# Kernel tuning notes

Hardware: AMD Instinct MI355X
Metric: run time of the kernel (lower is better)

Reference implementation:

```python
import jax, jax.numpy as jnp
import numpy as np

N, K, P, A, NBINS, RP = 4096, 48, 128, 5, 16, 32
LN_EPS = 1e-5

def _normalize(v, eps=1e-6):
    return v / jnp.sqrt(jnp.maximum((v * v).sum(-1, keepdims=True), eps))

def extract_frames(pos):
    # pos: [N, A, 3]; atom order N, CA, C, ... -> Gram-Schmidt backbone frame
    n, ca, c = pos[:, 0], pos[:, 1], pos[:, 2]
    e1 = _normalize(c - ca)
    v2 = n - ca
    e2 = _normalize(v2 - (v2 * e1).sum(-1, keepdims=True) * e1)
    e3 = jnp.cross(e1, e2)
    R = jnp.stack([e1, e2, e3], axis=-1)  # [N,3,3], columns = frame axes
    return R, ca

def distance_rbf(d, d_min=0.0, d_max=22.0, bins=NBINS):
    step = (d_max - d_min) / bins
    centers = d_min + step * jnp.arange(bins, dtype=d.dtype)
    return jnp.exp(-(((d[..., None] - centers) / step) ** 2))

def relpos_features(resi, chain, batch, neighbours):
    # clipped relative sequence position, extra class for cross-chain/batch pairs
    rel = jnp.clip(resi[neighbours] - resi[:, None], -RP, RP) + RP
    same = (chain[neighbours] == chain[:, None]) & (batch[neighbours] == batch[:, None])
    cls = jnp.where(same, rel, 2 * RP + 1)
    return jax.nn.one_hot(cls, 2 * RP + 2, dtype=jnp.float32)  # [N,K,66]

def distance_features(pos, neighbours):
    pn = pos[neighbours]  # [N,K,A,3] gather
    diff = pos[:, None, :, None] - pn[:, :, None, :]  # [N,K,A,A,3]
    d = jnp.sqrt(jnp.maximum((diff * diff).sum(-1), 1e-12))
    return distance_rbf(d).reshape(N, K, A * A * NBINS)

def direction_features(pos, neighbours, R, ca):
    rel = pos[neighbours] - ca[:, None, None]  # [N,K,A,3]
    local = jnp.einsum('nji,nkaj->nkai', R, rel)  # express in frame of residue i
    return _normalize(local).reshape(N, K, A * 3)

def rotation_features(neighbours, R):
    Rrel = jnp.einsum('nji,nkjl->nkil', R, R[neighbours])  # R_i^T R_j
    return Rrel.reshape(N, K, 9)

def pair_vector_features(pos, neighbours, R, ca):
    rel = pos[neighbours] - ca[:, None, None]
    local = jnp.einsum('nji,nkaj->nkai', R, rel)
    return local.reshape(N, K, A * 3)

def setup_inputs() -> dict:
    key = jax.random.key(0)
    ks = jax.random.split(key, 12)
    s = 0.02
    pos = 5.0 * jax.random.normal(ks[0], (N, A, 3), dtype=jnp.float32)
    dmap = 22.0 * jax.random.uniform(ks[1], (N, N), dtype=jnp.float32)
    mask = jnp.ones((N,), dtype=jnp.float32)
    neighbours = jax.random.randint(ks[2], (N, K), 0, N, dtype=jnp.int32)
    resi = jnp.arange(N, dtype=jnp.int32)
    chain = jnp.zeros((N,), dtype=jnp.int32)
    batch = jnp.zeros((N,), dtype=jnp.int32)
    W_relpos = s * jax.random.normal(ks[3], (2 * RP + 2, P), dtype=jnp.float32)
    W_dmap = s * jax.random.normal(ks[4], (NBINS, P), dtype=jnp.float32)
    W_dist = s * jax.random.normal(ks[5], (A * A * NBINS, P), dtype=jnp.float32)
    W_dir = s * jax.random.normal(ks[6], (3 * A, P), dtype=jnp.float32)
    W_rot = s * jax.random.normal(ks[7], (9, P), dtype=jnp.float32)
    W_vec = s * jax.random.normal(ks[8], (3 * A, P), dtype=jnp.float32)
    ln_scale = jnp.ones((P,), dtype=jnp.float32)
    ln_offset = jnp.zeros((P,), dtype=jnp.float32)
    W1 = s * jax.random.normal(ks[9], (P, 2 * P), dtype=jnp.float32)
    b1 = jnp.zeros((2 * P,), dtype=jnp.float32)
    W2 = s * jax.random.normal(ks[10], (2 * P, P), dtype=jnp.float32)
    b2 = jnp.zeros((P,), dtype=jnp.float32)
    return dict(pos=pos, dmap=dmap, mask=mask, W_relpos=W_relpos, W_dmap=W_dmap,
                W_dist=W_dist, W_dir=W_dir, W_rot=W_rot, W_vec=W_vec,
                ln_scale=ln_scale, ln_offset=ln_offset, W1=W1, b1=b1, W2=W2, b2=b2,
                neighbours=neighbours, resi=resi, chain=chain, batch=batch)

def reference(pos, dmap, mask, W_relpos, W_dmap, W_dist, W_dir, W_rot, W_vec,
              ln_scale, ln_offset, W1, b1, W2, b2, neighbours, resi, chain, batch):
    pair_mask = mask[:, None] * mask[neighbours] * (neighbours != -1).astype(mask.dtype)
    R, ca = extract_frames(pos)
    idx = jnp.arange(N)
    dmap_nb = dmap[idx[:, None], neighbours]  # [N,K] gather of distance map
    # multi-branch linear sum
    pair = relpos_features(resi, chain, batch, neighbours) @ W_relpos
    pair += jnp.where(pair_mask[..., None] > 0, distance_rbf(dmap_nb), 0.0) @ W_dmap
    pair += distance_features(pos, neighbours) @ W_dist
    pair += direction_features(pos, neighbours, R, ca) @ W_dir
    pair += rotation_features(neighbours, R) @ W_rot
    pair += pair_vector_features(pos, neighbours, R, ca) @ W_vec
    # LayerNorm (create_scale=True, create_offset=True)
    mu = pair.mean(-1, keepdims=True)
    var = ((pair - mu) ** 2).mean(-1, keepdims=True)
    pair = (pair - mu) / jnp.sqrt(var + LN_EPS) * ln_scale + ln_offset
    # MLP(2P -> P) with gelu
    pair = jax.nn.gelu(pair @ W1 + b1) @ W2 + b2
    return pair, pair_mask
```

## Files before the change

### kernel.cpp

```cpp
#include <hip/hip_runtime.h>
#include <hip/hip_bf16.h>

#define N_RES 4096
#define KNB   48
#define PCH   128
#define INV_STEP 0.727272727272727f
#define E2INV 0.13533528323661270f

typedef __bf16 bf16x8 __attribute__((ext_vector_type(8)));
typedef float  f32x4  __attribute__((ext_vector_type(4)));

__device__ __align__(16) unsigned short g_wcat[68*128*8];
__device__ __align__(16) unsigned short g_w1[16*256*8];
__device__ __align__(16) unsigned short g_w2[32*128*8];

__device__ __forceinline__ unsigned short f2bf(float f) {
  unsigned int u = __float_as_uint(f);
  return (unsigned short)((u + 0x7fffu + ((u >> 16) & 1u)) >> 16);
}
__device__ __forceinline__ unsigned int pk2(float a, float b) {
  __hip_bfloat162 h = __float22bfloat162_rn(make_float2(a, b));
  unsigned int u; __builtin_memcpy(&u, &h, 4); return u;
}
__device__ __forceinline__ float gelu_t(float x) {
  float u = 0.7978845608028654f * (x + 0.044715f * x * x * x);
  float a = fabsf(u);
  float e = __expf(-2.0f * a);
  float th = (1.0f - e) / (1.0f + e);
  th = (u < 0.0f) ? -th : th;
  return 0.5f * x * (1.0f + th);
}
__device__ __forceinline__ void frame_from_pos(const float* p, float* R) {
  float cax = p[3], cay = p[4], caz = p[5];
  float e1x = p[6]-cax, e1y = p[7]-cay, e1z = p[8]-caz;
  float i1 = 1.0f / sqrtf(fmaxf(e1x*e1x + e1y*e1y + e1z*e1z, 1e-6f));
  e1x *= i1; e1y *= i1; e1z *= i1;
  float vx = p[0]-cax, vy = p[1]-cay, vz = p[2]-caz;
  float dp = vx*e1x + vy*e1y + vz*e1z;
  float e2x = vx - dp*e1x, e2y = vy - dp*e1y, e2z = vz - dp*e1z;
  float i2 = 1.0f / sqrtf(fmaxf(e2x*e2x + e2y*e2y + e2z*e2z, 1e-6f));
  e2x *= i2; e2y *= i2; e2z *= i2;
  float e3x = e1y*e2z - e1z*e2y;
  float e3y = e1z*e2x - e1x*e2z;
  float e3z = e1x*e2y - e1y*e2x;
  R[0]=e1x; R[1]=e2x; R[2]=e3x;
  R[3]=e1y; R[4]=e2y; R[5]=e3y;
  R[6]=e1z; R[7]=e2z; R[8]=e3z;
}

__device__ __forceinline__ void stage_bins(unsigned short* sF, const float* s_xall,
                                           int xbase, int ntasks, int t) {
  for (int i = t; i < ntasks; i += 256) {
    int rloc = i / 48;
    int m = i - 48*rloc;
    float x = fminf(s_xall[(xbase + rloc)*48 + m], 25.0f);
    float u  = __expf(-x*x);
    float wu = __expf(2.0f*x - 1.0f);
    float xm = x - 15.0f;
    float d  = __expf(-xm*xm);
    float wd = __expf(-2.0f*xm - 1.0f);
    float bins[16];
    bins[0] = u;
    #pragma unroll
    for (int b = 1; b < 16; ++b) { u *= wu; wu *= E2INV; bins[b] = u; }
    bins[15] = fmaxf(bins[15], d);
    #pragma unroll
    for (int b = 14; b >= 0; --b) { d *= wd; wd *= E2INV; bins[b] = fmaxf(bins[b], d); }
    unsigned int p0 = pk2(bins[0], bins[1]),  p1 = pk2(bins[2], bins[3]);
    unsigned int p2 = pk2(bins[4], bins[5]),  p3 = pk2(bins[6], bins[7]);
    unsigned int p4 = pk2(bins[8], bins[9]),  p5 = pk2(bins[10], bins[11]);
    unsigned int p6 = pk2(bins[12], bins[13]),p7 = pk2(bins[14], bins[15]);
    int base = ((rloc*2)*48 + m)*8;
    *(uint4*)(sF + base)        = make_uint4(p0,p1,p2,p3);
    *(uint4*)(sF + base + 384)  = make_uint4(p4,p5,p6,p7);
  }
}

__global__ __launch_bounds__(256) void prep_weights(
    const float* __restrict__ W_relpos, const float* __restrict__ W_dmap,
    const float* __restrict__ W_dist, const float* __restrict__ W_dir,
    const float* __restrict__ W_rot, const float* __restrict__ W_vec,
    const float* __restrict__ W1, const float* __restrict__ W2)
{
  int i = blockIdx.x*256 + threadIdx.x;
  unsigned short pk[8];
  if (i < 8704) {
    int oct = i >> 7, col = i & 127;
    #pragma unroll
    for (int j = 0; j < 8; ++j) {
      int k = oct*8 + j;
      float v;
      if      (k < 16)  v = W_dmap[k*128 + col];
      else if (k < 416) v = W_dist[(k-16)*128 + col];
      else if (k < 431) v = W_dir[(k-416)*128 + col];
      else if (k < 446) v = W_vec[(k-431)*128 + col];
      else if (k < 455) v = W_rot[(k-446)*128 + col];
      else if (k < 521) v = W_relpos[(k-455)*128 + col];
      else              v = 0.0f;
      pk[j] = f2bf(v);
    }
    *(uint4*)(g_wcat + i*8) = *(uint4*)pk;
  } else if (i < 12800) {
    int j2 = i - 8704;
    int oct = j2 >> 8, col = j2 & 255;
    #pragma unroll
    for (int j = 0; j < 8; ++j) pk[j] = f2bf(W1[(oct*8+j)*256 + col]);
    *(uint4*)(g_w1 + j2*8) = *(uint4*)pk;
  } else if (i < 16896) {
    int j3 = i - 12800;
    int oct = j3 >> 7, col = j3 & 127;
    #pragma unroll
    for (int j = 0; j < 8; ++j) pk[j] = f2bf(W2[(oct*8+j)*128 + col]);
    *(uint4*)(g_w2 + j3*8) = *(uint4*)pk;
  }
}

#define MFMA6(A0,A1,A2,B0,B1,ACC) \
  ACC[0][0] = __builtin_amdgcn_mfma_f32_16x16x32_bf16(A0, B0, ACC[0][0], 0,0,0); \
  ACC[1][0] = __builtin_amdgcn_mfma_f32_16x16x32_bf16(A1, B0, ACC[1][0], 0,0,0); \
  ACC[2][0] = __builtin_amdgcn_mfma_f32_16x16x32_bf16(A2, B0, ACC[2][0], 0,0,0); \
  ACC[0][1] = __builtin_amdgcn_mfma_f32_16x16x32_bf16(A0, B1, ACC[0][1], 0,0,0); \
  ACC[1][1] = __builtin_amdgcn_mfma_f32_16x16x32_bf16(A1, B1, ACC[1][1], 0,0,0); \
  ACC[2][1] = __builtin_amdgcn_mfma_f32_16x16x32_bf16(A2, B1, ACC[2][1], 0,0,0);

__global__ __launch_bounds__(256, 5) void fused_struct_kernel(
    const float* __restrict__ pos, const float* __restrict__ dmap,
    const float* __restrict__ mask, const float* __restrict__ ln_scale,
    const float* __restrict__ ln_offset, const float* __restrict__ b1,
    const float* __restrict__ b2, const int* __restrict__ neighbours,
    const int* __restrict__ resi, const int* __restrict__ chain,
    const int* __restrict__ batch, float* __restrict__ out)
{
  const int n = blockIdx.x;
  const int t = threadIdx.x;
  const int lane = t & 63;
  const int wv   = t >> 6;
  const int ln15 = lane & 15;
  const int quad = lane >> 4;

  __shared__ __align__(16) char regF[12288];
  __shared__ __align__(16) char regP[12288];
  __shared__ __align__(16) float2 s_stats[48];

  unsigned short* sF    = (unsigned short*)regF;
  unsigned short* sPair = (unsigned short*)regP;
  float*  s_posnb = (float*)regP;
  float*  s_Rnb   = (float*)(regP + 3072);
  float*  s_xall  = (float*)(regP + 5376);
  float*  s_posn  = (float*)(regP + 10368);
  float*  s_Rn    = (float*)(regP + 10432);
  int*    s_cls   = (int*)  (regP + 10496);
  float2* s_part  = (float2*)(regP + 10752);

  if (t < KNB) {
    const int k = t;
    const int nbraw = neighbours[n*KNB + k];
    int nb = nbraw; if (nb < 0) nb += N_RES;
    float p[15];
    const float* pp = pos + nb*15;
    #pragma unroll
    for (int d = 0; d < 15; ++d) { p[d] = pp[d]; s_posnb[k*16+d] = p[d]; }
    float R[9];
    frame_from_pos(p, R);
    #pragma unroll
    for (int d = 0; d < 9; ++d) s_Rnb[k*12+d] = R[d];

    float pm = mask[n] * mask[nb] * ((nbraw != -1) ? 1.0f : 0.0f);
    out[N_RES*KNB*PCH + n*KNB + k] = pm;

    int rel = resi[nb] - resi[n];
    rel = (rel < -32) ? -32 : (rel > 32 ? 32 : rel);
    rel += 32;
    bool same = (chain[nb] == chain[n]) && (batch[nb] == batch[n]);
    s_cls[k] = same ? rel : 65;

    float xd = dmap[(long long)n*N_RES + nb] * INV_STEP;
    s_xall[k] = (pm > 0.0f) ? xd : 30.0f;
  } else if (t == 255) {
    float p[15];
    const float* pp = pos + n*15;
    #pragma unroll
    for (int d = 0; d < 15; ++d) { p[d] = pp[d]; s_posn[d] = p[d]; }
    float R[9];
    frame_from_pos(p, R);
    #pragma unroll
    for (int d = 0; d < 9; ++d) s_Rn[d] = R[d];
  }
  __syncthreads();

  for (int idx = t; idx < 1200; idx += 256) {
    int c = idx / 48, k = idx - 48*c;
    int a1 = c / 5, a2 = c - 5*a1;
    float dx = s_posn[a1*3+0] - s_posnb[k*16 + a2*3+0];
    float dy = s_posn[a1*3+1] - s_posnb[k*16 + a2*3+1];
    float dz = s_posn[a1*3+2] - s_posnb[k*16 + a2*3+2];
    float d2 = dx*dx + dy*dy + dz*dz;
    s_xall[48 + idx] = sqrtf(fmaxf(d2, 1e-12f)) * INV_STEP;
  }
  __syncthreads();

  f32x4 acc1[3][2] = {};

  #pragma unroll 1
  for (int st = 0; st < 3; ++st) {
    stage_bins(sF, s_xall, st*8, 384, t);
    __syncthreads();
    #pragma unroll
    for (int kc = 0; kc < 4; ++kc) {
      const unsigned short* ab = sF + ((kc*4 + quad)*48 + ln15)*8;
      bf16x8 a0 = *(const bf16x8*)(ab);
      bf16x8 a1 = *(const bf16x8*)(ab + 128);
      bf16x8 a2 = *(const bf16x8*)(ab + 256);
      const unsigned short* bb = g_wcat + (((st*4+kc)*4 + quad)*128 + 32*wv + ln15)*8;
      bf16x8 b0 = *(const bf16x8*)(bb);
      bf16x8 b1v= *(const bf16x8*)(bb + 128);
      MFMA6(a0,a1,a2,b0,b1v,acc1)
    }
    __syncthreads();
  }

  for (int i = t; i < 768; i += 256) ((uint4*)sF)[i] = make_uint4(0,0,0,0);
  __syncthreads();
  stage_bins(sF, s_xall, 24, 96, t);
  for (int idx = t; idx < 240; idx += 256) {
    int k = idx / 5, a = idx - 5*k;
    float rx = s_posnb[k*16 + a*3+0] - s_posn[3];
    float ry = s_posnb[k*16 + a*3+1] - s_posn[4];
    float rz = s_posnb[k*16 + a*3+2] - s_posn[5];
    float l0 = s_Rn[0]*rx + s_Rn[3]*ry + s_Rn[6]*rz;
    float l1 = s_Rn[1]*rx + s_Rn[4]*ry + s_Rn[7]*rz;
    float l2 = s_Rn[2]*rx + s_Rn[5]*ry + s_Rn[8]*rz;
    float inv = 1.0f / sqrtf(fmaxf(l0*l0 + l1*l1 + l2*l2, 1e-6f));
    int lv = 47 + a*3, ld = 32 + a*3;
    sF[((lv>>3)*48 + k)*8 + (lv&7)] = f2bf(l0);
    lv++; sF[((lv>>3)*48 + k)*8 + (lv&7)] = f2bf(l1);
    lv++; sF[((lv>>3)*48 + k)*8 + (lv&7)] = f2bf(l2);
    sF[((ld>>3)*48 + k)*8 + (ld&7)] = f2bf(l0*inv);
    ld++; sF[((ld>>3)*48 + k)*8 + (ld&7)] = f2bf(l1*inv);
    ld++; sF[((ld>>3)*48 + k)*8 + (ld&7)] = f2bf(l2*inv);
  }
  for (int idx = t; idx < 432; idx += 256) {
    int k = idx / 9, il = idx - 9*k;
    int i2 = il / 3, l2c = il - 3*i2;
    float v = s_Rn[0+i2]*s_Rnb[k*12 + 0+l2c]
            + s_Rn[3+i2]*s_Rnb[k*12 + 3+l2c]
            + s_Rn[6+i2]*s_Rnb[k*12 + 6+l2c];
    int l = 62 + il;
    sF[((l>>3)*48 + k)*8 + (l&7)] = f2bf(v);
  }
  if (t < 48) {
    int c = s_cls[t];
    if (c <= 56) { int l = 71 + c; sF[((l>>3)*48 + t)*8 + (l&7)] = 0x3F80; }
  }
  __syncthreads();
  #pragma unroll
  for (int kc = 0; kc < 4; ++kc) {
    const unsigned short* ab = sF + ((kc*4 + quad)*48 + ln15)*8;
    bf16x8 a0 = *(const bf16x8*)(ab);
    bf16x8 a1 = *(const bf16x8*)(ab + 128);
    bf16x8 a2 = *(const bf16x8*)(ab + 256);
    const unsigned short* bb = g_wcat + (((12+kc)*4 + quad)*128 + 32*wv + ln15)*8;
    bf16x8 b0 = *(const bf16x8*)(bb);
    bf16x8 b1v= *(const bf16x8*)(bb + 128);
    MFMA6(a0,a1,a2,b0,b1v,acc1)
  }
  __syncthreads();

  for (int i = t; i < 192; i += 256) ((uint4*)sF)[i] = make_uint4(0,0,0,0);
  __syncthreads();
  if (t < 48) {
    int c = s_cls[t];
    if (c >= 57) { int l = c - 57; sF[((l>>3)*48 + t)*8 + (l&7)] = 0x3F80; }
  }
  __syncthreads();
  {
    const unsigned short* ab = sF + (quad*48 + ln15)*8;
    bf16x8 a0 = *(const bf16x8*)(ab);
    bf16x8 a1 = *(const bf16x8*)(ab + 128);
    bf16x8 a2 = *(const bf16x8*)(ab + 256);
    const unsigned short* bb = g_wcat + ((64 + quad)*128 + 32*wv + ln15)*8;
    bf16x8 b0 = *(const bf16x8*)(bb);
    bf16x8 b1v= *(const bf16x8*)(bb + 128);
    MFMA6(a0,a1,a2,b0,b1v,acc1)
  }

  #pragma unroll
  for (int mt = 0; mt < 3; ++mt)
    #pragma unroll
    for (int r = 0; r < 4; ++r) {
      float a0v = acc1[mt][0][r], a1v = acc1[mt][1][r];
      float sv = a0v + a1v;
      float qv = a0v*a0v + a1v*a1v;
      #pragma unroll
      for (int msk = 1; msk < 16; msk <<= 1) {
        sv += __shfl_xor(sv, msk);
        qv += __shfl_xor(qv, msk);
      }
      if (ln15 == 0) s_part[wv*48 + mt*16 + quad*4 + r] = make_float2(sv, qv);
    }
  __syncthreads();
  if (t < 48) {
    float S = 0.0f, Q = 0.0f;
    #pragma unroll
    for (int w = 0; w < 4; ++w) { float2 p = s_part[w*48 + t]; S += p.x; Q += p.y; }
    float mu = S * (1.0f/128.0f);
    float var = Q * (1.0f/128.0f) - mu*mu;
    s_stats[t] = make_float2(mu, 1.0f / sqrtf(var + 1e-5f));
  }
  __syncthreads();
  {
    int c0 = 32*wv + ln15;
    float gg0 = ln_scale[c0],  gg1 = ln_scale[c0+16];
    float oo0 = ln_offset[c0], oo1 = ln_offset[c0+16];
    #pragma unroll
    for (int mt = 0; mt < 3; ++mt)
      #pragma unroll
      for (int r = 0; r < 4; ++r) {
        int row = mt*16 + quad*4 + r;
        float2 stt = s_stats[row];
        float v0 = (acc1[mt][0][r] - stt.x)*stt.y*gg0 + oo0;
        float v1 = (acc1[mt][1][r] - stt.x)*stt.y*gg1 + oo1;
        sPair[((c0>>3)*48 + row)*8 + (c0&7)] = f2bf(v0);
        int c1 = c0 + 16;
        sPair[((c1>>3)*48 + row)*8 + (c1&7)] = f2bf(v1);
      }
  }
  __syncthreads();

  f32x4 acc3[3][2] = {};
  #pragma unroll 1
  for (int half = 0; half < 2; ++half) {
    f32x4 acc2[3][2] = {};
    #pragma unroll
    for (int kc = 0; kc < 4; ++kc) {
      const unsigned short* ab = sPair + ((kc*4 + quad)*48 + ln15)*8;
      bf16x8 a0 = *(const bf16x8*)(ab);
      bf16x8 a1 = *(const bf16x8*)(ab + 128);
      bf16x8 a2 = *(const bf16x8*)(ab + 256);
      const unsigned short* bb = g_w1 + ((kc*4 + quad)*256 + half*128 + 32*wv + ln15)*8;
      bf16x8 b0 = *(const bf16x8*)(bb);
      bf16x8 b1v= *(const bf16x8*)(bb + 128);
      MFMA6(a0,a1,a2,b0,b1v,acc2)
    }
    __syncthreads();
    {
      int hc = half*128 + 32*wv + ln15;
      float bb0 = b1[hc], bb1 = b1[hc+16];
      int l0 = 32*wv + ln15, l1 = l0 + 16;
      #pragma unroll
      for (int mt = 0; mt < 3; ++mt)
        #pragma unroll
        for (int r = 0; r < 4; ++r) {
          int row = mt*16 + quad*4 + r;
          sF[((l0>>3)*48 + row)*8 + (l0&7)] = f2bf(gelu_t(acc2[mt][0][r] + bb0));
          sF[((l1>>3)*48 + row)*8 + (l1&7)] = f2bf(gelu_t(acc2[mt][1][r] + bb1));
        }
    }
    __syncthreads();
    #pragma unroll
    for (int kc = 0; kc < 4; ++kc) {
      const unsigned short* ab = sF + ((kc*4 + quad)*48 + ln15)*8;
      bf16x8 a0 = *(const bf16x8*)(ab);
      bf16x8 a1 = *(const bf16x8*)(ab + 128);
      bf16x8 a2 = *(const bf16x8*)(ab + 256);
      const unsigned short* bb = g_w2 + (((half*4 + kc)*4 + quad)*128 + 32*wv + ln15)*8;
      bf16x8 b0 = *(const bf16x8*)(bb);
      bf16x8 b1v= *(const bf16x8*)(bb + 128);
      MFMA6(a0,a1,a2,b0,b1v,acc3)
    }
  }

  {
    int c0 = 32*wv + ln15;
    float bo0 = b2[c0], bo1 = b2[c0+16];
    #pragma unroll
    for (int mt = 0; mt < 3; ++mt)
      #pragma unroll
      for (int r = 0; r < 4; ++r) {
        int row = mt*16 + quad*4 + r;
        out[(n*KNB + row)*PCH + c0]      = acc3[mt][0][r] + bo0;
        out[(n*KNB + row)*PCH + c0 + 16] = acc3[mt][1][r] + bo1;
      }
  }
}

extern "C" void kernel_launch(void* const* d_in, const int* in_sizes, int n_in,
                              void* d_out, int out_size, void* d_ws, size_t ws_size,
                              hipStream_t stream) {
  const float* pos       = (const float*)d_in[0];
  const float* dmap      = (const float*)d_in[1];
  const float* mask      = (const float*)d_in[2];
  const float* W_relpos  = (const float*)d_in[3];
  const float* W_dmap    = (const float*)d_in[4];
  const float* W_dist    = (const float*)d_in[5];
  const float* W_dir     = (const float*)d_in[6];
  const float* W_rot     = (const float*)d_in[7];
  const float* W_vec     = (const float*)d_in[8];
  const float* ln_scale  = (const float*)d_in[9];
  const float* ln_offset = (const float*)d_in[10];
  const float* W1        = (const float*)d_in[11];
  const float* b1        = (const float*)d_in[12];
  const float* W2        = (const float*)d_in[13];
  const float* b2        = (const float*)d_in[14];
  const int* neighbours  = (const int*)d_in[15];
  const int* resi        = (const int*)d_in[16];
  const int* chain       = (const int*)d_in[17];
  const int* batch       = (const int*)d_in[18];
  float* out = (float*)d_out;

  hipLaunchKernelGGL(prep_weights, dim3(66), dim3(256), 0, stream,
                     W_relpos, W_dmap, W_dist, W_dir, W_rot, W_vec, W1, W2);
  hipLaunchKernelGGL(fused_struct_kernel, dim3(N_RES), dim3(256), 0, stream,
                     pos, dmap, mask, ln_scale, ln_offset, b1, b2,
                     neighbours, resi, chain, batch, out);
}
```

Measured before the change: 289.2 us.

## Replace relpos one-hot GEMM with row gather, pad LDS rows, pack stores

```diff
diff --git a/kernel.cpp b/kernel.cpp
--- a/kernel.cpp
+++ b/kernel.cpp
@@ -10,7 +10,9 @@
 typedef __bf16 bf16x8 __attribute__((ext_vector_type(8)));
 typedef float  f32x4  __attribute__((ext_vector_type(4)));
 
-__device__ __align__(16) unsigned short g_wcat[68*128*8];
+#define FOCT(o,m) (((o)*49 + (m))*8)
+
+__device__ __align__(16) unsigned short g_wcat[60*128*8];
 __device__ __align__(16) unsigned short g_w1[16*256*8];
 __device__ __align__(16) unsigned short g_w2[32*128*8];
 
@@ -22,23 +24,22 @@
   __hip_bfloat162 h = __float22bfloat162_rn(make_float2(a, b));
   unsigned int u; __builtin_memcpy(&u, &h, 4); return u;
 }
-__device__ __forceinline__ float gelu_t(float x) {
-  float u = 0.7978845608028654f * (x + 0.044715f * x * x * x);
-  float a = fabsf(u);
-  float e = __expf(-2.0f * a);
-  float th = (1.0f - e) / (1.0f + e);
-  th = (u < 0.0f) ? -th : th;
-  return 0.5f * x * (1.0f + th);
+__device__ __forceinline__ float gelu_f(float x) {
+  float p = x * x;
+  float q = fmaf(p, 0.044715f, 1.0f);
+  float r = x * q;
+  float e = __expf(-1.5957691216057308f * r);
+  return x * __builtin_amdgcn_rcpf(1.0f + e);
 }
 __device__ __forceinline__ void frame_from_pos(const float* p, float* R) {
   float cax = p[3], cay = p[4], caz = p[5];
   float e1x = p[6]-cax, e1y = p[7]-cay, e1z = p[8]-caz;
-  float i1 = 1.0f / sqrtf(fmaxf(e1x*e1x + e1y*e1y + e1z*e1z, 1e-6f));
+  float i1 = __builtin_amdgcn_rsqf(fmaxf(e1x*e1x + e1y*e1y + e1z*e1z, 1e-6f));
   e1x *= i1; e1y *= i1; e1z *= i1;
   float vx = p[0]-cax, vy = p[1]-cay, vz = p[2]-caz;
   float dp = vx*e1x + vy*e1y + vz*e1z;
   float e2x = vx - dp*e1x, e2y = vy - dp*e1y, e2z = vz - dp*e1z;
-  float i2 = 1.0f / sqrtf(fmaxf(e2x*e2x + e2y*e2y + e2z*e2z, 1e-6f));
+  float i2 = __builtin_amdgcn_rsqf(fmaxf(e2x*e2x + e2y*e2y + e2z*e2z, 1e-6f));
   e2x *= i2; e2y *= i2; e2z *= i2;
   float e3x = e1y*e2z - e1z*e2y;
   float e3y = e1z*e2x - e1x*e2z;
@@ -70,21 +71,21 @@
     unsigned int p2 = pk2(bins[4], bins[5]),  p3 = pk2(bins[6], bins[7]);
     unsigned int p4 = pk2(bins[8], bins[9]),  p5 = pk2(bins[10], bins[11]);
     unsigned int p6 = pk2(bins[12], bins[13]),p7 = pk2(bins[14], bins[15]);
-    int base = ((rloc*2)*48 + m)*8;
-    *(uint4*)(sF + base)        = make_uint4(p0,p1,p2,p3);
-    *(uint4*)(sF + base + 384)  = make_uint4(p4,p5,p6,p7);
+    int base = FOCT(2*rloc, m);
+    *(uint4*)(sF + base)       = make_uint4(p0,p1,p2,p3);
+    *(uint4*)(sF + base + 392) = make_uint4(p4,p5,p6,p7);
   }
 }
 
 __global__ __launch_bounds__(256) void prep_weights(
-    const float* __restrict__ W_relpos, const float* __restrict__ W_dmap,
-    const float* __restrict__ W_dist, const float* __restrict__ W_dir,
-    const float* __restrict__ W_rot, const float* __restrict__ W_vec,
-    const float* __restrict__ W1, const float* __restrict__ W2)
+    const float* __restrict__ W_dmap, const float* __restrict__ W_dist,
+    const float* __restrict__ W_dir, const float* __restrict__ W_rot,
+    const float* __restrict__ W_vec, const float* __restrict__ W1,
+    const float* __restrict__ W2)
 {
   int i = blockIdx.x*256 + threadIdx.x;
   unsigned short pk[8];
-  if (i < 8704) {
+  if (i < 7680) {
     int oct = i >> 7, col = i & 127;
     #pragma unroll
     for (int j = 0; j < 8; ++j) {
@@ -95,22 +96,30 @@
       else if (k < 431) v = W_dir[(k-416)*128 + col];
       else if (k < 446) v = W_vec[(k-431)*128 + col];
       else if (k < 455) v = W_rot[(k-446)*128 + col];
-      else if (k < 521) v = W_relpos[(k-455)*128 + col];
       else              v = 0.0f;
       pk[j] = f2bf(v);
     }
     *(uint4*)(g_wcat + i*8) = *(uint4*)pk;
-  } else if (i < 12800) {
-    int j2 = i - 8704;
+  } else if (i < 11776) {
+    int j2 = i - 7680;
     int oct = j2 >> 8, col = j2 & 255;
     #pragma unroll
-    for (int j = 0; j < 8; ++j) pk[j] = f2bf(W1[(oct*8+j)*256 + col]);
+    for (int j = 0; j < 8; ++j) {
+      int k = oct*8 + j;
+      int h = 32*(k>>5) + (k&1)*16 + ((k&31)>>1);
+      pk[j] = f2bf(W1[h*256 + col]);
+    }
     *(uint4*)(g_w1 + j2*8) = *(uint4*)pk;
-  } else if (i < 16896) {
-    int j3 = i - 12800;
+  } else if (i < 15872) {
+    int j3 = i - 11776;
     int oct = j3 >> 7, col = j3 & 127;
     #pragma unroll
-    for (int j = 0; j < 8; ++j) pk[j] = f2bf(W2[(oct*8+j)*128 + col]);
+    for (int j = 0; j < 8; ++j) {
+      int k = oct*8 + j;
+      int kh = k & 127;
+      int h = (k>>7)*128 + 32*(kh>>5) + (kh&1)*16 + ((kh&31)>>1);
+      pk[j] = f2bf(W2[h*128 + col]);
+    }
     *(uint4*)(g_w2 + j3*8) = *(uint4*)pk;
   }
 }
@@ -123,13 +132,14 @@
   ACC[1][1] = __builtin_amdgcn_mfma_f32_16x16x32_bf16(A1, B1, ACC[1][1], 0,0,0); \
   ACC[2][1] = __builtin_amdgcn_mfma_f32_16x16x32_bf16(A2, B1, ACC[2][1], 0,0,0);
 
-__global__ __launch_bounds__(256, 5) void fused_struct_kernel(
+__global__ __launch_bounds__(256, 6) void fused_struct_kernel(
     const float* __restrict__ pos, const float* __restrict__ dmap,
-    const float* __restrict__ mask, const float* __restrict__ ln_scale,
-    const float* __restrict__ ln_offset, const float* __restrict__ b1,
-    const float* __restrict__ b2, const int* __restrict__ neighbours,
-    const int* __restrict__ resi, const int* __restrict__ chain,
-    const int* __restrict__ batch, float* __restrict__ out)
+    const float* __restrict__ mask, const float* __restrict__ W_relpos,
+    const float* __restrict__ ln_scale, const float* __restrict__ ln_offset,
+    const float* __restrict__ b1, const float* __restrict__ b2,
+    const int* __restrict__ neighbours, const int* __restrict__ resi,
+    const int* __restrict__ chain, const int* __restrict__ batch,
+    float* __restrict__ out)
 {
   const int n = blockIdx.x;
   const int t = threadIdx.x;
@@ -138,8 +148,8 @@
   const int ln15 = lane & 15;
   const int quad = lane >> 4;
 
-  __shared__ __align__(16) char regF[12288];
-  __shared__ __align__(16) char regP[12288];
+  __shared__ __align__(16) char regF[12544];
+  __shared__ __align__(16) char regP[12544];
   __shared__ __align__(16) float2 s_stats[48];
 
   unsigned short* sF    = (unsigned short*)regF;
@@ -207,7 +217,7 @@
     __syncthreads();
     #pragma unroll
     for (int kc = 0; kc < 4; ++kc) {
-      const unsigned short* ab = sF + ((kc*4 + quad)*48 + ln15)*8;
+      const unsigned short* ab = sF + FOCT(kc*4 + quad, ln15);
       bf16x8 a0 = *(const bf16x8*)(ab);
       bf16x8 a1 = *(const bf16x8*)(ab + 128);
       bf16x8 a2 = *(const bf16x8*)(ab + 256);
@@ -219,8 +229,7 @@
     __syncthreads();
   }
 
-  for (int i = t; i < 768; i += 256) ((uint4*)sF)[i] = make_uint4(0,0,0,0);
-  __syncthreads();
+  for (int i = t; i < 147; i += 256) ((uint4*)sF)[441 + i] = make_uint4(0,0,0,0);
   stage_bins(sF, s_xall, 24, 96, t);
   for (int idx = t; idx < 240; idx += 256) {
     int k = idx / 5, a = idx - 5*k;
@@ -230,32 +239,31 @@
     float l0 = s_Rn[0]*rx + s_Rn[3]*ry + s_Rn[6]*rz;
     float l1 = s_Rn[1]*rx + s_Rn[4]*ry + s_Rn[7]*rz;
     float l2 = s_Rn[2]*rx + s_Rn[5]*ry + s_Rn[8]*rz;
-    float inv = 1.0f / sqrtf(fmaxf(l0*l0 + l1*l1 + l2*l2, 1e-6f));
+    float inv = __builtin_amdgcn_rsqf(fmaxf(l0*l0 + l1*l1 + l2*l2, 1e-6f));
     int lv = 47 + a*3, ld = 32 + a*3;
-    sF[((lv>>3)*48 + k)*8 + (lv&7)] = f2bf(l0);
-    lv++; sF[((lv>>3)*48 + k)*8 + (lv&7)] = f2bf(l1);
-    lv++; sF[((lv>>3)*48 + k)*8 + (lv&7)] = f2bf(l2);
-    sF[((ld>>3)*48 + k)*8 + (ld&7)] = f2bf(l0*inv);
-    ld++; sF[((ld>>3)*48 + k)*8 + (ld&7)] = f2bf(l1*inv);
-    ld++; sF[((ld>>3)*48 + k)*8 + (ld&7)] = f2bf(l2*inv);
-  }
-  for (int idx = t; idx < 432; idx += 256) {
-    int k = idx / 9, il = idx - 9*k;
-    int i2 = il / 3, l2c = il - 3*i2;
-    float v = s_Rn[0+i2]*s_Rnb[k*12 + 0+l2c]
-            + s_Rn[3+i2]*s_Rnb[k*12 + 3+l2c]
-            + s_Rn[6+i2]*s_Rnb[k*12 + 6+l2c];
+    sF[FOCT(lv>>3,k) + (lv&7)] = f2bf(l0);
+    lv++; sF[FOCT(lv>>3,k) + (lv&7)] = f2bf(l1);
+    lv++; sF[FOCT(lv>>3,k) + (lv&7)] = f2bf(l2);
+    sF[FOCT(ld>>3,k) + (ld&7)] = f2bf(l0*inv);
+    ld++; sF[FOCT(ld>>3,k) + (ld&7)] = f2bf(l1*inv);
+    ld++; sF[FOCT(ld>>3,k) + (ld&7)] = f2bf(l2*inv);
+  }
+  for (int idx = t; idx < 480; idx += 256) {
+    int k = idx / 10, il = idx - 10*k;
+    float v = 0.0f;
+    if (il < 9) {
+      int i2 = il / 3, l2c = il - 3*i2;
+      v = s_Rn[0+i2]*s_Rnb[k*12 + 0+l2c]
+        + s_Rn[3+i2]*s_Rnb[k*12 + 3+l2c]
+        + s_Rn[6+i2]*s_Rnb[k*12 + 6+l2c];
+    }
     int l = 62 + il;
-    sF[((l>>3)*48 + k)*8 + (l&7)] = f2bf(v);
-  }
-  if (t < 48) {
-    int c = s_cls[t];
-    if (c <= 56) { int l = 71 + c; sF[((l>>3)*48 + t)*8 + (l&7)] = 0x3F80; }
+    sF[FOCT(l>>3,k) + (l&7)] = f2bf(v);
   }
   __syncthreads();
   #pragma unroll
-  for (int kc = 0; kc < 4; ++kc) {
-    const unsigned short* ab = sF + ((kc*4 + quad)*48 + ln15)*8;
+  for (int kc = 0; kc < 3; ++kc) {
+    const unsigned short* ab = sF + FOCT(kc*4 + quad, ln15);
     bf16x8 a0 = *(const bf16x8*)(ab);
     bf16x8 a1 = *(const bf16x8*)(ab + 128);
     bf16x8 a2 = *(const bf16x8*)(ab + 256);
@@ -264,24 +272,18 @@
     bf16x8 b1v= *(const bf16x8*)(bb + 128);
     MFMA6(a0,a1,a2,b0,b1v,acc1)
   }
-  __syncthreads();
-
-  for (int i = t; i < 192; i += 256) ((uint4*)sF)[i] = make_uint4(0,0,0,0);
-  __syncthreads();
-  if (t < 48) {
-    int c = s_cls[t];
-    if (c >= 57) { int l = c - 57; sF[((l>>3)*48 + t)*8 + (l&7)] = 0x3F80; }
-  }
-  __syncthreads();
+
   {
-    const unsigned short* ab = sF + (quad*48 + ln15)*8;
-    bf16x8 a0 = *(const bf16x8*)(ab);
-    bf16x8 a1 = *(const bf16x8*)(ab + 128);
-    bf16x8 a2 = *(const bf16x8*)(ab + 256);
-    const unsigned short* bb = g_wcat + ((64 + quad)*128 + 32*wv + ln15)*8;
-    bf16x8 b0 = *(const bf16x8*)(bb);
-    bf16x8 b1v= *(const bf16x8*)(bb + 128);
-    MFMA6(a0,a1,a2,b0,b1v,acc1)
+    int c0 = 32*wv + ln15;
+    #pragma unroll
+    for (int mt = 0; mt < 3; ++mt)
+      #pragma unroll
+      for (int r = 0; r < 4; ++r) {
+        int row = mt*16 + quad*4 + r;
+        const float* wr = W_relpos + s_cls[row]*128 + c0;
+        acc1[mt][0][r] += wr[0];
+        acc1[mt][1][r] += wr[16];
+      }
   }
 
   #pragma unroll
@@ -305,13 +307,15 @@
     for (int w = 0; w < 4; ++w) { float2 p = s_part[w*48 + t]; S += p.x; Q += p.y; }
     float mu = S * (1.0f/128.0f);
     float var = Q * (1.0f/128.0f) - mu*mu;
-    s_stats[t] = make_float2(mu, 1.0f / sqrtf(var + 1e-5f));
+    s_stats[t] = make_float2(mu, __builtin_amdgcn_rsqf(var + 1e-5f));
   }
   __syncthreads();
   {
     int c0 = 32*wv + ln15;
     float gg0 = ln_scale[c0],  gg1 = ln_scale[c0+16];
     float oo0 = ln_offset[c0], oo1 = ln_offset[c0+16];
+    int kp = 32*wv + 2*ln15;
+    int oct = kp >> 3, slot = kp & 7;
     #pragma unroll
     for (int mt = 0; mt < 3; ++mt)
       #pragma unroll
@@ -320,9 +324,7 @@
         float2 stt = s_stats[row];
         float v0 = (acc1[mt][0][r] - stt.x)*stt.y*gg0 + oo0;
         float v1 = (acc1[mt][1][r] - stt.x)*stt.y*gg1 + oo1;
-        sPair[((c0>>3)*48 + row)*8 + (c0&7)] = f2bf(v0);
-        int c1 = c0 + 16;
-        sPair[((c1>>3)*48 + row)*8 + (c1&7)] = f2bf(v1);
+        *(unsigned int*)(sPair + FOCT(oct,row) + slot) = pk2(v0, v1);
       }
   }
   __syncthreads();
@@ -333,7 +335,7 @@
     f32x4 acc2[3][2] = {};
     #pragma unroll
     for (int kc = 0; kc < 4; ++kc) {
-      const unsigned short* ab = sPair + ((kc*4 + quad)*48 + ln15)*8;
+      const unsigned short* ab = sPair + FOCT(kc*4 + quad, ln15);
       bf16x8 a0 = *(const bf16x8*)(ab);
       bf16x8 a1 = *(const bf16x8*)(ab + 128);
       bf16x8 a2 = *(const bf16x8*)(ab + 256);
@@ -346,20 +348,22 @@
     {
       int hc = half*128 + 32*wv + ln15;
       float bb0 = b1[hc], bb1 = b1[hc+16];
-      int l0 = 32*wv + ln15, l1 = l0 + 16;
+      int kp = 32*wv + 2*ln15;
+      int oct = kp >> 3, slot = kp & 7;
       #pragma unroll
       for (int mt = 0; mt < 3; ++mt)
         #pragma unroll
         for (int r = 0; r < 4; ++r) {
           int row = mt*16 + quad*4 + r;
-          sF[((l0>>3)*48 + row)*8 + (l0&7)] = f2bf(gelu_t(acc2[mt][0][r] + bb0));
-          sF[((l1>>3)*48 + row)*8 + (l1&7)] = f2bf(gelu_t(acc2[mt][1][r] + bb1));
+          float h0 = gelu_f(acc2[mt][0][r] + bb0);
+          float h1 = gelu_f(acc2[mt][1][r] + bb1);
+          *(unsigned int*)(sF + FOCT(oct,row) + slot) = pk2(h0, h1);
         }
     }
     __syncthreads();
     #pragma unroll
     for (int kc = 0; kc < 4; ++kc) {
-      const unsigned short* ab = sF + ((kc*4 + quad)*48 + ln15)*8;
+      const unsigned short* ab = sF + FOCT(kc*4 + quad, ln15);
       bf16x8 a0 = *(const bf16x8*)(ab);
       bf16x8 a1 = *(const bf16x8*)(ab + 128);
       bf16x8 a2 = *(const bf16x8*)(ab + 256);
@@ -408,9 +412,9 @@
   const int* batch       = (const int*)d_in[18];
   float* out = (float*)d_out;
 
-  hipLaunchKernelGGL(prep_weights, dim3(66), dim3(256), 0, stream,
-                     W_relpos, W_dmap, W_dist, W_dir, W_rot, W_vec, W1, W2);
+  hipLaunchKernelGGL(prep_weights, dim3(62), dim3(256), 0, stream,
+                     W_dmap, W_dist, W_dir, W_rot, W_vec, W1, W2);
   hipLaunchKernelGGL(fused_struct_kernel, dim3(N_RES), dim3(256), 0, stream,
-                     pos, dmap, mask, ln_scale, ln_offset, b1, b2,
+                     pos, dmap, mask, W_relpos, ln_scale, ln_offset, b1, b2,
                      neighbours, resi, chain, batch, out);
 }
```

New measurement: 276.4 us. -4.4%, faster.
